# Kernel tuning notes

Hardware: AMD Instinct MI355X
Metric: run time of the kernel (lower is better)

Reference implementation:

```python
import jax, jax.numpy as jnp
import numpy as np

K = 3          # kernel_size
STRIDE = 1
PAD = 1
DIL = 1


def conv2d(x, w, b, stride=STRIDE, pad=PAD, dil=DIL):
    y = jax.lax.conv_general_dilated(
        x, w, window_strides=(stride, stride),
        padding=((pad, pad), (pad, pad)), rhs_dilation=(dil, dil),
        dimension_numbers=('NCHW', 'OIHW', 'NCHW'))
    if b is not None:
        y = y + b[None, :, None, None]
    return y


def bilinear_gather(x, py, px):
    """Zero-padded bilinear sampling.
    x: [B,C,H,W]; py,px: [B,K2,Ho,Wo] float coords. Returns [B,C,K2,Ho,Wo].
    Matches torchvision deform_conv2d: out-of-range corners contribute zero."""
    B, C, H, W = x.shape
    y0 = jnp.floor(py)
    x0 = jnp.floor(px)
    wy1 = py - y0
    wx1 = px - x0
    wy0 = 1.0 - wy1
    wx0 = 1.0 - wx1
    xf = x.reshape(B, C, H * W)

    def corner(yi, xi, wgt):
        valid = (yi >= 0) & (yi < H) & (xi >= 0) & (xi < W)
        yc = jnp.clip(yi, 0, H - 1).astype(jnp.int32)
        xc = jnp.clip(xi, 0, W - 1).astype(jnp.int32)
        idx = (yc * W + xc).reshape(B, 1, -1)            # [B,1,K2*Ho*Wo]
        v = jnp.take_along_axis(xf, idx, axis=2)         # [B,C,K2*Ho*Wo]
        v = v.reshape(B, C, *yi.shape[1:])               # [B,C,K2,Ho,Wo]
        w = (wgt * valid.astype(x.dtype))[:, None]       # [B,1,K2,Ho,Wo]
        return v * w

    return (corner(y0, x0, wy0 * wx0) + corner(y0, x0 + 1, wy0 * wx1)
            + corner(y0 + 1, x0, wy1 * wx0) + corner(y0 + 1, x0 + 1, wy1 * wx1))


def reference(x, w_offset, b_offset, w_mask, b_mask, w_deform):
    B, C, H, W = x.shape
    K2 = K * K
    offset = conv2d(x, w_offset, b_offset)               # [B,2*K2,Ho,Wo]
    mask = jax.nn.sigmoid(conv2d(x, w_mask, b_mask))     # [B,K2,Ho,Wo]
    Ho, Wo = offset.shape[2], offset.shape[3]

    off = offset.reshape(B, K2, 2, Ho, Wo)
    dy, dx = off[:, :, 0], off[:, :, 1]                  # [B,K2,Ho,Wo]

    ky = (jnp.arange(K2) // K).astype(x.dtype) * DIL     # kernel tap row offsets
    kx = (jnp.arange(K2) % K).astype(x.dtype) * DIL
    base_y = (jnp.arange(Ho) * STRIDE - PAD).astype(x.dtype)
    base_x = (jnp.arange(Wo) * STRIDE - PAD).astype(x.dtype)
    py = dy + base_y[None, None, :, None] + ky[None, :, None, None]
    px = dx + base_x[None, None, None, :] + kx[None, :, None, None]

    val = bilinear_gather(x, py, px)                     # [B,C,K2,Ho,Wo]
    val = val * mask[:, None]                            # modulation

    w = w_deform.reshape(w_deform.shape[0], C, K2)       # [Cout,Cin,K2]
    return jnp.einsum('bckhw,ock->bohw', val, w)


def setup_inputs() -> dict:
    key = jax.random.key(0)
    k = jax.random.split(key, 6)
    B, Cin, Cout, H, W = 2, 64, 64, 224, 224
    x = jax.random.normal(k[0], (B, Cin, H, W), dtype=jnp.float32)
    # source zero-inits offset/mask convs; use small random weights to exercise
    # fractional, scattered sampling coordinates.
    w_offset = jax.random.normal(k[1], (2 * K * K, Cin, K, K), dtype=jnp.float32) * 0.01
    b_offset = jnp.zeros((2 * K * K,), dtype=jnp.float32)
    w_mask = jax.random.normal(k[2], (K * K, Cin, K, K), dtype=jnp.float32) * 0.01
    b_mask = jnp.zeros((K * K,), dtype=jnp.float32)
    w_deform = jax.random.normal(k[3], (Cout, Cin, K, K), dtype=jnp.float32) * (1.0 / np.sqrt(Cin * K * K))
    return {"x": x, "w_offset": w_offset, "b_offset": b_offset,
            "w_mask": w_mask, "b_mask": b_mask, "w_deform": w_deform}
```

## Files before the change

### kernel.cpp

```cpp
#include <hip/hip_runtime.h>
#include <hip/hip_bf16.h>
#include <math.h>

constexpr int B    = 2;
constexpr int C    = 64;
constexpr int H    = 224;
constexpr int W    = 224;
constexpr int Hp   = 226;
constexpr int Wp   = 226;
constexpr int K2   = 9;
constexpr int OCO  = 18;
constexpr int OM   = 27;
constexpr int COUT = 64;
constexpr int HW   = H * W;
constexpr int NPIX = B * HW;
constexpr int CK   = C * K2;
constexpr int CPB  = 32;

typedef short  bf16x8 __attribute__((ext_vector_type(8)));
typedef float  f32x4  __attribute__((ext_vector_type(4)));

__device__ inline unsigned short f2bf(float f) {
    union { float f; unsigned u; } v; v.f = f;
    unsigned r = v.u + 0x7FFF + ((v.u >> 16) & 1);
    return (unsigned short)(r >> 16);
}
__device__ inline unsigned cvtpk(float a, float b) {
    __hip_bfloat162 h = __float22bfloat162_rn(make_float2(a, b));
    union { __hip_bfloat162 h; unsigned u; } cv; cv.h = h;
    return cv.u;
}
__device__ inline float blo(unsigned u) { union { unsigned u; float f; } c; c.u = u << 16; return c.f; }
__device__ inline float bhi(unsigned u) { union { unsigned u; float f; } c; c.u = u & 0xFFFF0000u; return c.f; }

__global__ __launch_bounds__(256) void k_padT(const float* __restrict__ x,
                                              unsigned short* __restrict__ xp) {
    __shared__ float tile[64][33];
    const int b   = blockIdx.y;
    const int hw0 = blockIdx.x * 32;
    const int tid = threadIdx.x;
    const int hwl = tid & 31, cl = tid >> 5;
    const float* xb = x + (size_t)b * C * HW;
#pragma unroll
    for (int j = 0; j < 8; ++j) {
        int c = cl + j * 8;
        tile[c][hwl] = xb[(size_t)c * HW + hw0 + hwl];
    }
    __syncthreads();
    unsigned short* xpb = xp + (size_t)b * Hp * Wp * C;
    const int l15 = tid & 15, hh = tid >> 4;
    const int c = l15 * 4;
    {
        int hw = hw0 + hh;
        int y = hw / W, xx = hw % W;
        float t0 = tile[c][hh], t1 = tile[c + 1][hh];
        float t2 = tile[c + 2][hh], t3 = tile[c + 3][hh];
        *reinterpret_cast<uint2*>(xpb + ((size_t)(y + 1) * Wp + (xx + 1)) * C + c) =
            make_uint2(cvtpk(t0, t1), cvtpk(t2, t3));
    }
    {
        int hw = hw0 + 16 + hh;
        int y = hw / W, xx = hw % W;
        float t0 = tile[c][16 + hh], t1 = tile[c + 1][16 + hh];
        float t2 = tile[c + 2][16 + hh], t3 = tile[c + 3][16 + hh];
        *reinterpret_cast<uint2*>(xpb + ((size_t)(y + 1) * Wp + (xx + 1)) * C + c) =
            make_uint2(cvtpk(t0, t1), cvtpk(t2, t3));
    }
}

__global__ void k_border(unsigned short* __restrict__ xp) {
    int i = blockIdx.x * 256 + threadIdx.x;
    if (i >= B * 900 * 8) return;
    int chunk = i & 7;
    int cell  = (i >> 3) % 900;
    int b     = (i >> 3) / 900;
    int y, x;
    if      (cell < 226) { y = 0;              x = cell; }
    else if (cell < 452) { y = Hp - 1;         x = cell - 226; }
    else if (cell < 676) { y = cell - 452 + 1; x = 0; }
    else                 { y = cell - 676 + 1; x = Wp - 1; }
    uint4 z = make_uint4(0u, 0u, 0u, 0u);
    *reinterpret_cast<uint4*>(xp + ((size_t)b * Hp * Wp + y * Wp + x) * C + chunk * 8) = z;
}

__global__ void k_wA(const float* __restrict__ wd, unsigned short* __restrict__ wA) {
    int i = blockIdx.x * 256 + threadIdx.x;
    if (i >= COUT * CK) return;
    int o  = i / CK;
    int kc = i % CK;
    int k  = kc >> 6;
    int c  = kc & 63;
    wA[i] = f2bf(wd[((size_t)o * C + c) * 9 + k]);
}

__global__ void k_womA(const float* __restrict__ w_off,
                       const float* __restrict__ w_msk,
                       const float* __restrict__ b_off,
                       const float* __restrict__ b_msk,
                       unsigned short* __restrict__ womA,
                       float* __restrict__ biasv) {
    int i = blockIdx.x * 256 + threadIdx.x;
    if (i < 32) biasv[i] = (i < OCO) ? b_off[i] : (i < OM) ? b_msk[i - OCO] : 0.f;
    if (i >= 32 * CK) return;
    int oc = i / CK;
    int kc = i % CK;
    int k  = kc >> 6;
    int c  = kc & 63;
    float v = (oc < OCO) ? w_off[((size_t)oc * C + c) * 9 + k]
            : (oc < OM)  ? w_msk[((size_t)(oc - OCO) * C + c) * 9 + k]
                         : 0.f;
    womA[i] = f2bf(v);
}

__global__ __launch_bounds__(256, 4) void k_convom(const unsigned short* __restrict__ xp,
                                                   const unsigned short* __restrict__ womA,
                                                   const float* __restrict__ biasv,
                                                   int4* __restrict__ gtabO,
                                                   float4* __restrict__ gtabW) {
    __shared__ __align__(16) unsigned short imcol[CPB * CK];
    __shared__ float som[CPB][28];
    const int tid  = threadIdx.x;
    const int lane = tid & 63;
    const int wv   = tid >> 6;
    const int q    = lane >> 4;
    const int l15  = lane & 15;
    int bid = blockIdx.x;
    bid = (bid & 7) * (gridDim.x >> 3) + (bid >> 3);
    const int pix0 = bid * CPB;
    const int bb   = pix0 / HW;
    const unsigned short* xb = xp + (size_t)bb * Hp * Wp * C;

    const int c0 = l15 * 4;
#pragma unroll
    for (int pi = 0; pi < 2; ++pi) {
        const int p_local = pi * 16 + wv * 4 + q;
        const int pix = pix0 + p_local;
        const int hw  = pix - bb * HW;
        const int y   = hw / W;
        const int xx  = hw % W;
        int wbase = p_local * (CK * 2) + l15 * 8;
        wbase ^= (p_local & 7) << 4;
#pragma unroll
        for (int k = 0; k < 9; ++k) {
            const int ky = k / 3, kx = k % 3;
            const uint2 v = *reinterpret_cast<const uint2*>(
                xb + ((size_t)(y + ky) * Wp + (xx + kx)) * C + c0);
            *reinterpret_cast<uint2*>(reinterpret_cast<char*>(imcol) + wbase + k * 128) = v;
        }
    }
    __syncthreads();

    f32x4 acc = {0.f, 0.f, 0.f, 0.f};
    const int m = wv & 1, n = wv >> 1;
    const unsigned short* a0 = womA + (size_t)(m * 16 + l15) * CK;
    const int row = n * 16 + l15;
#pragma unroll 3
    for (int ks = 0; ks < 18; ++ks) {
        int byte = row * (CK * 2) + ks * 64 + q * 16;
        byte ^= (row & 7) << 4;
        const bf16x8 bfv = *reinterpret_cast<const bf16x8*>(
            reinterpret_cast<const char*>(imcol) + byte);
        const bf16x8 af = *reinterpret_cast<const bf16x8*>(a0 + ks * 32 + q * 8);
        acc = __builtin_amdgcn_mfma_f32_16x16x32_bf16(af, bfv, acc, 0, 0, 0);
    }

    {
        const int p = n * 16 + l15;
#pragma unroll
        for (int r = 0; r < 4; ++r) {
            const int oc = m * 16 + q * 4 + r;
            if (oc < OM) {
                float v = acc[r] + biasv[oc];
                som[p][oc] = (oc < OCO) ? v : 1.0f / (1.0f + __expf(-v));
            }
        }
    }
    __syncthreads();

    for (int e = tid; e < CPB * 9; e += 256) {
        const int p  = e / 9;
        const int k  = e - p * 9;
        const int pix = pix0 + p;
        const int hw  = pix - bb * HW;
        const int ho  = hw / W;
        const int wo  = hw - ho * W;
        const int ky  = k / 3, kx = k - (k / 3) * 3;
        const float dy = som[p][2 * k];
        const float dx = som[p][2 * k + 1];
        const float mm = som[p][OCO + k];
        const float py = dy + (float)(ho + ky - 1);
        const float px = dx + (float)(wo + kx - 1);
        const float fy = floorf(py), fx = floorf(px);
        const int   y0 = (int)fy,   x0 = (int)fx;
        const float wy1 = py - fy,  wx1 = px - fx;
        const float wy0 = 1.f - wy1, wx0 = 1.f - wx1;
        const bool iy0 = (y0 >= 0) & (y0 < H);
        const bool iy1 = (y0 + 1 >= 0) & (y0 + 1 < H);
        const bool ix0 = (x0 >= 0) & (x0 < W);
        const bool ix1 = (x0 + 1 >= 0) & (x0 + 1 < W);
        const int ya = min(max(y0 + 1, 0), Hp - 1);
        const int yb = min(max(y0 + 2, 0), Hp - 1);
        const int xa = min(max(x0 + 1, 0), Wp - 1);
        const int xc = min(max(x0 + 2, 0), Wp - 1);
        const int rA = ya * Wp, rB = yb * Wp;
        gtabO[(size_t)pix * 9 + k] = make_int4((rA + xa) * C, (rA + xc) * C,
                                               (rB + xa) * C, (rB + xc) * C);
        gtabW[(size_t)pix * 9 + k] = make_float4(
            wy0 * wx0 * mm * ((iy0 & ix0) ? 1.f : 0.f),
            wy0 * wx1 * mm * ((iy0 & ix1) ? 1.f : 0.f),
            wy1 * wx0 * mm * ((iy1 & ix0) ? 1.f : 0.f),
            wy1 * wx1 * mm * ((iy1 & ix1) ? 1.f : 0.f));
    }
}

__global__ __launch_bounds__(256, 4) void k_deform(const unsigned short* __restrict__ xp,
                                                   const int4* __restrict__ gtabO,
                                                   const float4* __restrict__ gtabW,
                                                   const unsigned short* __restrict__ wA,
                                                   float* __restrict__ out) {
    __shared__ __align__(16) unsigned short valT[CPB * CK];
    const int tid  = threadIdx.x;
    const int lane = tid & 63;
    const int wv   = tid >> 6;
    const int q    = lane >> 4;
    const int l15  = lane & 15;
    int bid = blockIdx.x;
    bid = (bid & 7) * (gridDim.x >> 3) + (bid >> 3);
    const int pix0 = bid * CPB;
    const int bb   = pix0 / HW;
    const unsigned short* xb = xp + (size_t)bb * Hp * Wp * C;

    const int c0 = l15 * 4;
#pragma unroll
    for (int pi = 0; pi < 2; ++pi) {
        const int p_local = pi * 16 + wv * 4 + q;
        const int pix = pix0 + p_local;
        const int4*   gO = gtabO + (size_t)pix * 9;
        const float4* gW = gtabW + (size_t)pix * 9;
        int wbase = p_local * (CK * 2) + l15 * 8;
        wbase ^= (p_local & 7) << 4;
#pragma unroll
        for (int k = 0; k < 9; ++k) {
            const int4   o  = gO[k];
            const float4 wt = gW[k];
            const uint2 u00 = *reinterpret_cast<const uint2*>(xb + o.x + c0);
            const uint2 u01 = *reinterpret_cast<const uint2*>(xb + o.y + c0);
            const uint2 u10 = *reinterpret_cast<const uint2*>(xb + o.z + c0);
            const uint2 u11 = *reinterpret_cast<const uint2*>(xb + o.w + c0);
            const float s0 = wt.x * blo(u00.x) + wt.y * blo(u01.x) + wt.z * blo(u10.x) + wt.w * blo(u11.x);
            const float s1 = wt.x * bhi(u00.x) + wt.y * bhi(u01.x) + wt.z * bhi(u10.x) + wt.w * bhi(u11.x);
            const float s2 = wt.x * blo(u00.y) + wt.y * blo(u01.y) + wt.z * blo(u10.y) + wt.w * blo(u11.y);
            const float s3 = wt.x * bhi(u00.y) + wt.y * bhi(u01.y) + wt.z * bhi(u10.y) + wt.w * bhi(u11.y);
            *reinterpret_cast<uint2*>(reinterpret_cast<char*>(valT) + wbase + k * 128) =
                make_uint2(cvtpk(s0, s1), cvtpk(s2, s3));
        }
    }
    __syncthreads();

    f32x4 acc[2] = {{0.f,0.f,0.f,0.f},{0.f,0.f,0.f,0.f}};
    const unsigned short* wrow = wA + (size_t)(wv * 16 + l15) * CK;
#pragma unroll 3
    for (int ks = 0; ks < 18; ++ks) {
        const bf16x8 af = *reinterpret_cast<const bf16x8*>(wrow + ks * 32 + q * 8);
#pragma unroll
        for (int nt = 0; nt < 2; ++nt) {
            const int row = nt * 16 + l15;
            int byte = row * (CK * 2) + ks * 64 + q * 16;
            byte ^= (row & 7) << 4;
            const bf16x8 bfv = *reinterpret_cast<const bf16x8*>(
                reinterpret_cast<const char*>(valT) + byte);
            acc[nt] = __builtin_amdgcn_mfma_f32_16x16x32_bf16(af, bfv, acc[nt], 0, 0, 0);
        }
    }

    const int o0 = wv * 16 + q * 4;
#pragma unroll
    for (int nt = 0; nt < 2; ++nt) {
        const int pixn = pix0 + nt * 16 + l15;
        const int hw   = pixn - bb * HW;
#pragma unroll
        for (int r = 0; r < 4; ++r)
            out[((size_t)bb * COUT + o0 + r) * HW + hw] = acc[nt][r];
    }
}

extern "C" void kernel_launch(void* const* d_in, const int* in_sizes, int n_in,
                              void* d_out, int out_size, void* d_ws, size_t ws_size,
                              hipStream_t stream) {
    const float* x     = (const float*)d_in[0];
    const float* w_off = (const float*)d_in[1];
    const float* b_off = (const float*)d_in[2];
    const float* w_msk = (const float*)d_in[3];
    const float* b_msk = (const float*)d_in[4];
    const float* w_def = (const float*)d_in[5];
    float* out = (float*)d_out;

    unsigned short* xpadT = (unsigned short*)d_ws;
    int4*   gtabO = (int4*)(xpadT + (size_t)B * Hp * Wp * C);
    float4* gtabW = (float4*)(gtabO + (size_t)NPIX * 9);
    float*  biasv = (float*)(gtabW + (size_t)NPIX * 9);
    unsigned short* wA   = (unsigned short*)(biasv + 32);
    unsigned short* womA = wA + (size_t)COUT * CK;

    k_border<<<(B * 900 * 8 + 255) / 256, 256, 0, stream>>>(xpadT);
    k_padT<<<dim3(HW / 32, B), 256, 0, stream>>>(x, xpadT);
    k_wA<<<(COUT * CK + 255) / 256, 256, 0, stream>>>(w_def, wA);
    k_womA<<<(32 * CK + 255) / 256, 256, 0, stream>>>(w_off, w_msk, b_off, b_msk,
                                                      womA, biasv);
    k_convom<<<NPIX / CPB, 256, 0, stream>>>(xpadT, womA, biasv, gtabO, gtabW);
    k_deform<<<NPIX / CPB, 256, 0, stream>>>(xpadT, gtabO, gtabW, wA, out);
}
```

Before: 200.7 us.

## Fuse offset/mask conv and deformable gather-GEMM into one kernel

Merges k_convom and k_deform into a single kernel. The per-pixel sampling plan (corner offsets and modulated bilinear weights) now stays in shared memory instead of going through global gtabO/gtabW tables, and the im2col LDS buffer is reused for the deformed values. This removes the global write and reread of the tables and one kernel launch. In exchange, LDS use per block rises and launch bounds drop from 4 to 3 blocks per CU, which can lower occupancy. There is also an extra barrier between stages.

```diff
diff --git a/kernel.cpp b/kernel.cpp
--- a/kernel.cpp
+++ b/kernel.cpp
@@ -8,13 +8,12 @@
 constexpr int W    = 224;
 constexpr int Hp   = 226;
 constexpr int Wp   = 226;
-constexpr int K2   = 9;
 constexpr int OCO  = 18;
 constexpr int OM   = 27;
 constexpr int COUT = 64;
 constexpr int HW   = H * W;
 constexpr int NPIX = B * HW;
-constexpr int CK   = C * K2;
+constexpr int CK   = C * 9;
 constexpr int CPB  = 32;
 
 typedef short  bf16x8 __attribute__((ext_vector_type(8)));
@@ -50,19 +49,12 @@
     unsigned short* xpb = xp + (size_t)b * Hp * Wp * C;
     const int l15 = tid & 15, hh = tid >> 4;
     const int c = l15 * 4;
-    {
-        int hw = hw0 + hh;
+#pragma unroll
+    for (int half = 0; half < 2; ++half) {
+        int hw = hw0 + half * 16 + hh;
         int y = hw / W, xx = hw % W;
-        float t0 = tile[c][hh], t1 = tile[c + 1][hh];
-        float t2 = tile[c + 2][hh], t3 = tile[c + 3][hh];
-        *reinterpret_cast<uint2*>(xpb + ((size_t)(y + 1) * Wp + (xx + 1)) * C + c) =
-            make_uint2(cvtpk(t0, t1), cvtpk(t2, t3));
-    }
-    {
-        int hw = hw0 + 16 + hh;
-        int y = hw / W, xx = hw % W;
-        float t0 = tile[c][16 + hh], t1 = tile[c + 1][16 + hh];
-        float t2 = tile[c + 2][16 + hh], t3 = tile[c + 3][16 + hh];
+        float t0 = tile[c][half * 16 + hh],     t1 = tile[c + 1][half * 16 + hh];
+        float t2 = tile[c + 2][half * 16 + hh], t3 = tile[c + 3][half * 16 + hh];
         *reinterpret_cast<uint2*>(xpb + ((size_t)(y + 1) * Wp + (xx + 1)) * C + c) =
             make_uint2(cvtpk(t0, t1), cvtpk(t2, t3));
     }
@@ -112,13 +104,15 @@
     womA[i] = f2bf(v);
 }
 
-__global__ __launch_bounds__(256, 4) void k_convom(const unsigned short* __restrict__ xp,
-                                                   const unsigned short* __restrict__ womA,
-                                                   const float* __restrict__ biasv,
-                                                   int4* __restrict__ gtabO,
-                                                   float4* __restrict__ gtabW) {
+__global__ __launch_bounds__(256, 3) void k_fused(const unsigned short* __restrict__ xp,
+                                                  const unsigned short* __restrict__ womA,
+                                                  const unsigned short* __restrict__ wA,
+                                                  const float* __restrict__ biasv,
+                                                  float* __restrict__ out) {
     __shared__ __align__(16) unsigned short imcol[CPB * CK];
     __shared__ float som[CPB][28];
+    __shared__ int4   gplanO[CPB * 9];
+    __shared__ float4 gplanW[CPB * 9];
     const int tid  = threadIdx.x;
     const int lane = tid & 63;
     const int wv   = tid >> 6;
@@ -131,6 +125,7 @@
     const unsigned short* xb = xp + (size_t)bb * Hp * Wp * C;
 
     const int c0 = l15 * 4;
+
 #pragma unroll
     for (int pi = 0; pi < 2; ++pi) {
         const int p_local = pi * 16 + wv * 4 + q;
@@ -150,44 +145,43 @@
     }
     __syncthreads();
 
-    f32x4 acc = {0.f, 0.f, 0.f, 0.f};
-    const int m = wv & 1, n = wv >> 1;
-    const unsigned short* a0 = womA + (size_t)(m * 16 + l15) * CK;
-    const int row = n * 16 + l15;
+    {
+        f32x4 acc = {0.f, 0.f, 0.f, 0.f};
+        const int m = wv & 1, n = wv >> 1;
+        const unsigned short* a0 = womA + (size_t)(m * 16 + l15) * CK;
+        const int row = n * 16 + l15;
 #pragma unroll 3
-    for (int ks = 0; ks < 18; ++ks) {
-        int byte = row * (CK * 2) + ks * 64 + q * 16;
-        byte ^= (row & 7) << 4;
-        const bf16x8 bfv = *reinterpret_cast<const bf16x8*>(
-            reinterpret_cast<const char*>(imcol) + byte);
-        const bf16x8 af = *reinterpret_cast<const bf16x8*>(a0 + ks * 32 + q * 8);
-        acc = __builtin_amdgcn_mfma_f32_16x16x32_bf16(af, bfv, acc, 0, 0, 0);
-    }
-
-    {
-        const int p = n * 16 + l15;
+        for (int ks = 0; ks < 18; ++ks) {
+            int byte = row * (CK * 2) + ks * 64 + q * 16;
+            byte ^= (row & 7) << 4;
+            const bf16x8 bfv = *reinterpret_cast<const bf16x8*>(
+                reinterpret_cast<const char*>(imcol) + byte);
+            const bf16x8 af = *reinterpret_cast<const bf16x8*>(a0 + ks * 32 + q * 8);
+            acc = __builtin_amdgcn_mfma_f32_16x16x32_bf16(af, bfv, acc, 0, 0, 0);
+        }
+        const int pp = n * 16 + l15;
 #pragma unroll
         for (int r = 0; r < 4; ++r) {
             const int oc = m * 16 + q * 4 + r;
             if (oc < OM) {
                 float v = acc[r] + biasv[oc];
-                som[p][oc] = (oc < OCO) ? v : 1.0f / (1.0f + __expf(-v));
+                som[pp][oc] = (oc < OCO) ? v : 1.0f / (1.0f + __expf(-v));
             }
         }
     }
     __syncthreads();
 
     for (int e = tid; e < CPB * 9; e += 256) {
-        const int p  = e / 9;
-        const int k  = e - p * 9;
-        const int pix = pix0 + p;
+        const int pe = e / 9;
+        const int k  = e - pe * 9;
+        const int pix = pix0 + pe;
         const int hw  = pix - bb * HW;
         const int ho  = hw / W;
         const int wo  = hw - ho * W;
         const int ky  = k / 3, kx = k - (k / 3) * 3;
-        const float dy = som[p][2 * k];
-        const float dx = som[p][2 * k + 1];
-        const float mm = som[p][OCO + k];
+        const float dy = som[pe][2 * k];
+        const float dx = som[pe][2 * k + 1];
+        const float mm = som[pe][OCO + k];
         const float py = dy + (float)(ho + ky - 1);
         const float px = dx + (float)(wo + kx - 1);
         const float fy = floorf(py), fx = floorf(px);
@@ -203,46 +197,25 @@
         const int xa = min(max(x0 + 1, 0), Wp - 1);
         const int xc = min(max(x0 + 2, 0), Wp - 1);
         const int rA = ya * Wp, rB = yb * Wp;
-        gtabO[(size_t)pix * 9 + k] = make_int4((rA + xa) * C, (rA + xc) * C,
-                                               (rB + xa) * C, (rB + xc) * C);
-        gtabW[(size_t)pix * 9 + k] = make_float4(
+        gplanO[e] = make_int4((rA + xa) * C, (rA + xc) * C,
+                              (rB + xa) * C, (rB + xc) * C);
+        gplanW[e] = make_float4(
             wy0 * wx0 * mm * ((iy0 & ix0) ? 1.f : 0.f),
             wy0 * wx1 * mm * ((iy0 & ix1) ? 1.f : 0.f),
             wy1 * wx0 * mm * ((iy1 & ix0) ? 1.f : 0.f),
             wy1 * wx1 * mm * ((iy1 & ix1) ? 1.f : 0.f));
     }
-}
-
-__global__ __launch_bounds__(256, 4) void k_deform(const unsigned short* __restrict__ xp,
-                                                   const int4* __restrict__ gtabO,
-                                                   const float4* __restrict__ gtabW,
-                                                   const unsigned short* __restrict__ wA,
-                                                   float* __restrict__ out) {
-    __shared__ __align__(16) unsigned short valT[CPB * CK];
-    const int tid  = threadIdx.x;
-    const int lane = tid & 63;
-    const int wv   = tid >> 6;
-    const int q    = lane >> 4;
-    const int l15  = lane & 15;
-    int bid = blockIdx.x;
-    bid = (bid & 7) * (gridDim.x >> 3) + (bid >> 3);
-    const int pix0 = bid * CPB;
-    const int bb   = pix0 / HW;
-    const unsigned short* xb = xp + (size_t)bb * Hp * Wp * C;
-
-    const int c0 = l15 * 4;
+    __syncthreads();
+
 #pragma unroll
     for (int pi = 0; pi < 2; ++pi) {
         const int p_local = pi * 16 + wv * 4 + q;
-        const int pix = pix0 + p_local;
-        const int4*   gO = gtabO + (size_t)pix * 9;
-        const float4* gW = gtabW + (size_t)pix * 9;
         int wbase = p_local * (CK * 2) + l15 * 8;
         wbase ^= (p_local & 7) << 4;
 #pragma unroll
         for (int k = 0; k < 9; ++k) {
-            const int4   o  = gO[k];
-            const float4 wt = gW[k];
+            const int4   o  = gplanO[p_local * 9 + k];
+            const float4 wt = gplanW[p_local * 9 + k];
             const uint2 u00 = *reinterpret_cast<const uint2*>(xb + o.x + c0);
             const uint2 u01 = *reinterpret_cast<const uint2*>(xb + o.y + c0);
             const uint2 u10 = *reinterpret_cast<const uint2*>(xb + o.z + c0);
@@ -251,7 +224,7 @@
             const float s1 = wt.x * bhi(u00.x) + wt.y * bhi(u01.x) + wt.z * bhi(u10.x) + wt.w * bhi(u11.x);
             const float s2 = wt.x * blo(u00.y) + wt.y * blo(u01.y) + wt.z * blo(u10.y) + wt.w * blo(u11.y);
             const float s3 = wt.x * bhi(u00.y) + wt.y * bhi(u01.y) + wt.z * bhi(u10.y) + wt.w * bhi(u11.y);
-            *reinterpret_cast<uint2*>(reinterpret_cast<char*>(valT) + wbase + k * 128) =
+            *reinterpret_cast<uint2*>(reinterpret_cast<char*>(imcol) + wbase + k * 128) =
                 make_uint2(cvtpk(s0, s1), cvtpk(s2, s3));
         }
     }
@@ -268,7 +241,7 @@
             int byte = row * (CK * 2) + ks * 64 + q * 16;
             byte ^= (row & 7) << 4;
             const bf16x8 bfv = *reinterpret_cast<const bf16x8*>(
-                reinterpret_cast<const char*>(valT) + byte);
+                reinterpret_cast<const char*>(imcol) + byte);
             acc[nt] = __builtin_amdgcn_mfma_f32_16x16x32_bf16(af, bfv, acc[nt], 0, 0, 0);
         }
     }
@@ -296,9 +269,7 @@
     float* out = (float*)d_out;
 
     unsigned short* xpadT = (unsigned short*)d_ws;
-    int4*   gtabO = (int4*)(xpadT + (size_t)B * Hp * Wp * C);
-    float4* gtabW = (float4*)(gtabO + (size_t)NPIX * 9);
-    float*  biasv = (float*)(gtabW + (size_t)NPIX * 9);
+    float* biasv = (float*)(xpadT + (size_t)B * Hp * Wp * C);
     unsigned short* wA   = (unsigned short*)(biasv + 32);
     unsigned short* womA = wA + (size_t)COUT * CK;
 
@@ -307,6 +278,5 @@
     k_wA<<<(COUT * CK + 255) / 256, 256, 0, stream>>>(w_def, wA);
     k_womA<<<(32 * CK + 255) / 256, 256, 0, stream>>>(w_off, w_msk, b_off, b_msk,
                                                       womA, biasv);
-    k_convom<<<NPIX / CPB, 256, 0, stream>>>(xpadT, womA, biasv, gtabO, gtabW);
-    k_deform<<<NPIX / CPB, 256, 0, stream>>>(xpadT, gtabO, gtabW, wA, out);
-}
+    k_fused<<<NPIX / CPB, 256, 0, stream>>>(xpadT, womA, wA, biasv, out);
+}
```

Measured after the change: 183.8 us. -8.4%, faster.
